# Kernel optimization log

Measured on AMD Instinct MI355X. Metric: run time of the kernel, lower is better.

The kernel has to match this reference:

```python
import jax, jax.numpy as jnp
import numpy as np


def _conv1x1(x, w, b):
    # x: (B,C,H,W), w: (O,C), b: (O,)
    return jnp.einsum('bchw,oc->bohw', x, w) + b[None, :, None, None]


def setup_inputs() -> dict:
    key = jax.random.key(0)
    ks = jax.random.split(key, 10)
    B, C, H, W = 8, 64, 64, 64
    x = jax.random.normal(ks[0], (B, C, H, W), dtype=jnp.float32)
    s = 0.05
    params = {}
    names = ['wq', 'wQ', 'wK', 'wV']
    for i, n in enumerate(names):
        params[n] = jax.random.normal(ks[1 + 2 * i], (C, C), dtype=jnp.float32) * s
        params['b' + n[1:]] = jax.random.normal(ks[2 + 2 * i], (C,), dtype=jnp.float32) * s
    return dict(x=x, wq=params['wq'], bq=params['bq'], wQ=params['wQ'], bQ=params['bQ'],
                wK=params['wK'], bK=params['bK'], wV=params['wV'], bV=params['bV'],
                gamma=jnp.ones((1,), dtype=jnp.float32))


def reference(x, wq, bq, wQ, bQ, wK, bK, wV, bV, gamma):
    B, C, H, W = x.shape
    # q = query_conv(x).view(B,-1,W,H)  (pure reshape, matches torch .view on contiguous tensor)
    q = _conv1x1(x, wq, bq).reshape(B, C, W, H)
    # 2x2 average pool, stride 2
    qp = q.reshape(B, C, W // 2, 2, H // 2, 2).mean(axis=(3, 5))
    q_ = qp.reshape(B, C, (W * H) // 4)          # (B, C, N/4)
    K = _conv1x1(x, wK, bK).reshape(B, C, H * W)  # (B, C, N)
    V = _conv1x1(x, wV, bV).reshape(B, C, H * W)  # (B, C, N)
    # stage 1: pooled queries attend over all keys
    attn1 = jax.nn.softmax(jnp.einsum('bcp,bcn->bpn', q_, K), axis=-1)  # (B, N/4, N)
    out = jnp.einsum('bcn,bpn->bcp', V, attn1)                           # (B, C, N/4)
    # stage 2: full queries attend over pooled anchors
    Q = _conv1x1(x, wQ, bQ).reshape(B, C, H * W)                         # (B, C, N)
    attn2 = jax.nn.softmax(jnp.einsum('bcn,bcp->bnp', Q, q_), axis=-1)   # (B, N, N/4)
    out = jnp.einsum('bcp,bnp->bcn', out, attn2)                         # (B, C, N)
    out = out.reshape(B, C, H, W)
    return gamma * out + x
```

## Files before the change

kernel.cpp:

```cpp
#include <hip/hip_runtime.h>
#include <hip/hip_bf16.h>


typedef float  f32x4  __attribute__((ext_vector_type(4)));
typedef __bf16 bf16x8 __attribute__((ext_vector_type(8)));
typedef __bf16 bf16x4 __attribute__((ext_vector_type(4)));

__device__ __forceinline__ int swz(int ch) { return ch ^ ((ch >> 3) & 7); }

__global__ __launch_bounds__(256) void conv4_kernel(
    const float* __restrict__ x,
    const float* __restrict__ wq, const float* __restrict__ bq,
    const float* __restrict__ wQ, const float* __restrict__ bQ,
    const float* __restrict__ wK, const float* __restrict__ bK,
    const float* __restrict__ wV, const float* __restrict__ bV,
    __bf16* __restrict__ Kt, __bf16* __restrict__ Vc,
    __bf16* __restrict__ Qt, __bf16* __restrict__ qt)
{
  __shared__ float xs[64 * 132];
  __shared__ float wsh[64 * 68];

  const int tid = threadIdx.x;
  const int m   = blockIdx.x >> 8;
  const int b   = (blockIdx.x >> 5) & 7;
  const int rp  = blockIdx.x & 31;
  const int n0  = rp << 7;

  const float* wg = (m == 0) ? wK : (m == 1) ? wV : (m == 2) ? wQ : wq;
  const float* bg = (m == 0) ? bK : (m == 1) ? bV : (m == 2) ? bQ : bq;

  for (int i = tid; i < 64 * 32; i += 256) {
    int c = i >> 5, j = i & 31;
    *(f32x4*)&xs[c * 132 + j * 4] =
        *(const f32x4*)&x[((size_t)(b * 64 + c)) * 4096 + n0 + j * 4];
  }
  for (int i = tid; i < 1024; i += 256) {
    int o = i >> 4, c0 = (i & 15) << 2;
    f32x4 v = *(const f32x4*)&wg[o * 64 + c0];
    wsh[(c0 + 0) * 68 + o] = v[0];
    wsh[(c0 + 1) * 68 + o] = v[1];
    wsh[(c0 + 2) * 68 + o] = v[2];
    wsh[(c0 + 3) * 68 + o] = v[3];
  }
  __syncthreads();

  const int ty = tid >> 4, tx = tid & 15;

  float acc[4][8];
  {
    f32x4 bv = *(const f32x4*)&bg[ty * 4];
#pragma unroll
    for (int i = 0; i < 4; ++i)
#pragma unroll
      for (int j = 0; j < 8; ++j) acc[i][j] = bv[i];
  }

#pragma unroll 4
  for (int c = 0; c < 64; ++c) {
    f32x4 wv = *(const f32x4*)&wsh[c * 68 + ty * 4];
    f32x4 xa = *(const f32x4*)&xs[c * 132 + tx * 8];
    f32x4 xb = *(const f32x4*)&xs[c * 132 + tx * 8 + 4];
#pragma unroll
    for (int i = 0; i < 4; ++i) {
#pragma unroll
      for (int j = 0; j < 4; ++j) {
        acc[i][j]     += wv[i] * xa[j];
        acc[i][j + 4] += wv[i] * xb[j];
      }
    }
  }

  if (m == 0 || m == 2) {
    __bf16* dst = (m == 0) ? Kt : Qt;
#pragma unroll
    for (int j = 0; j < 8; ++j) {
      int n = n0 + tx * 8 + j;
      bf16x4 pk;
#pragma unroll
      for (int i = 0; i < 4; ++i) pk[i] = (__bf16)acc[i][j];
      *(bf16x4*)&dst[((size_t)(b * 4096 + n)) * 64 + ty * 4] = pk;
    }
  } else if (m == 1) {
#pragma unroll
    for (int i = 0; i < 4; ++i) {
      int o = ty * 4 + i;
      bf16x8 pk;
#pragma unroll
      for (int j = 0; j < 8; ++j) pk[j] = (__bf16)acc[i][j];
      *(bf16x8*)&Vc[((size_t)(b * 64 + o)) * 4096 + n0 + tx * 8] = pk;
    }
  } else {
    float pl[4][4];
#pragma unroll
    for (int i = 0; i < 4; ++i)
#pragma unroll
      for (int jj = 0; jj < 4; ++jj)
        pl[i][jj] = acc[i][2 * jj] + acc[i][2 * jj + 1];
#pragma unroll
    for (int i = 0; i < 4; ++i)
#pragma unroll
      for (int jj = 0; jj < 4; ++jj)
        pl[i][jj] += __shfl_xor(pl[i][jj], 8);
    if (tx < 8) {
#pragma unroll
      for (int jj = 0; jj < 4; ++jj) {
        int p = rp * 32 + tx * 4 + jj;
        bf16x4 pk;
#pragma unroll
        for (int i = 0; i < 4; ++i) pk[i] = (__bf16)(0.25f * pl[i][jj]);
        *(bf16x4*)&qt[((size_t)(b * 1024 + p)) * 64 + ty * 4] = pk;
      }
    }
  }
}

template <int NQB, int NKS, int KVLEN>
__global__ __launch_bounds__(512, 2) void attn_part_kernel(
    const __bf16* __restrict__ Qg,
    const __bf16* __restrict__ Kg,
    const __bf16* __restrict__ Vg,
    __bf16* __restrict__ partOb,
    float* __restrict__ partL)
{
  __shared__ __align__(16) char smem[65536];
  constexpr int RND = KVLEN / (NKS * 64);

  const int tid = threadIdx.x;
  const int w = tid >> 6, lane = tid & 63;
  const int lg = (lane >> 4) & 3, lp = lane & 15;
  const int b   = blockIdx.x / (NQB * NKS);
  const int rem = blockIdx.x % (NQB * NKS);
  const int qb  = rem / NKS;
  const int ks  = rem % NKS;

  bf16x8 qf[2][2];
#pragma unroll
  for (int qs = 0; qs < 2; ++qs) {
    const __bf16* qg =
        Qg + ((size_t)(b * (NQB * 256) + qb * 256 + w * 32 + qs * 16 + lp)) * 64;
    qf[qs][0] = *(const bf16x8*)(qg + lg * 8);
    qf[qs][1] = *(const bf16x8*)(qg + 32 + lg * 8);
  }

  f32x4 acc[2][4];
#pragma unroll
  for (int qs = 0; qs < 2; ++qs)
#pragma unroll
    for (int ct = 0; ct < 4; ++ct) acc[qs][ct] = (f32x4){0.f, 0.f, 0.f, 0.f};
  float l_run[2] = {0.f, 0.f};

  bf16x8 kreg, vreg;
  const int swt = swz(tid);
  auto load_tile = [&](int r) {
    const int kv0 = ks * (KVLEN / NKS) + r * 64;
    kreg = *(const bf16x8*)(Kg + ((size_t)(b * KVLEN + kv0 + (tid >> 3))) * 64 +
                            (tid & 7) * 8);
    vreg = *(const bf16x8*)(Vg + ((size_t)(b * 64 + (tid >> 3))) * KVLEN + kv0 +
                            (tid & 7) * 8);
  };
  auto write_tile = [&](int nb) {
    *(bf16x8*)((__bf16*)(smem + nb * 8192) + swt * 8) = kreg;
    *(bf16x8*)((__bf16*)(smem + 16384 + nb * 8192) + swt * 8) = vreg;
  };

  load_tile(0); write_tile(0); load_tile(1);
  __syncthreads();

  for (int r = 0; r < RND; ++r) {
    const int cur = r & 1;
    if (r + 1 < RND) write_tile(cur ^ 1);
    if (r + 2 < RND) load_tile(r + 2);

    const __bf16* lK = (const __bf16*)(smem + cur * 8192);
    const __bf16* lV = (const __bf16*)(smem + 16384 + cur * 8192);
    __bf16* lP = (__bf16*)(smem + 32768) + w * 2048;

    bf16x8 ka[4][2];
#pragma unroll
    for (int mt = 0; mt < 4; ++mt) {
      int ch0 = (mt * 16 + lp) * 8 + lg;
      ka[mt][0] = *(const bf16x8*)(lK + swz(ch0) * 8);
      ka[mt][1] = *(const bf16x8*)(lK + swz(ch0 + 4) * 8);
    }

#pragma unroll
    for (int qs = 0; qs < 2; ++qs) {
      f32x4 S[4];
#pragma unroll
      for (int mt = 0; mt < 4; ++mt) {
        f32x4 z = (f32x4){0.f, 0.f, 0.f, 0.f};
        z = __builtin_amdgcn_mfma_f32_16x16x32_bf16(ka[mt][0], qf[qs][0], z, 0, 0, 0);
        z = __builtin_amdgcn_mfma_f32_16x16x32_bf16(ka[mt][1], qf[qs][1], z, 0, 0, 0);
        S[mt] = z;
      }

      float rs = 0.f;
#pragma unroll
      for (int mt = 0; mt < 4; ++mt)
#pragma unroll
        for (int rr = 0; rr < 4; ++rr) {
          float e = __expf(S[mt][rr]);
          S[mt][rr] = e;
          rs += e;
        }
      rs += __shfl_xor(rs, 16);
      rs += __shfl_xor(rs, 32);
      l_run[qs] += rs;

#pragma unroll
      for (int mt = 0; mt < 4; ++mt) {
        bf16x4 pk;
#pragma unroll
        for (int rr = 0; rr < 4; ++rr) pk[rr] = (__bf16)S[mt][rr];
        int boff = (qs * 16 + lp) * 128 + mt * 32 + lg * 8;
        *(bf16x4*)((char*)lP + (boff ^ ((lp & 7) << 4))) = pk;
      }
    }

    bf16x8 pf[2][2];
#pragma unroll
    for (int qs = 0; qs < 2; ++qs) {
      int chp = (qs * 16 + lp) * 8 + lg;
      pf[qs][0] = *(const bf16x8*)(lP + swz(chp) * 8);
      pf[qs][1] = *(const bf16x8*)(lP + swz(chp + 4) * 8);
    }
#pragma unroll
    for (int ct = 0; ct < 4; ++ct) {
      int chv = (ct * 16 + lp) * 8 + lg;
      bf16x8 v0 = *(const bf16x8*)(lV + swz(chv) * 8);
      bf16x8 v1 = *(const bf16x8*)(lV + swz(chv + 4) * 8);
#pragma unroll
      for (int qs = 0; qs < 2; ++qs) {
        acc[qs][ct] = __builtin_amdgcn_mfma_f32_16x16x32_bf16(v0, pf[qs][0], acc[qs][ct], 0, 0, 0);
        acc[qs][ct] = __builtin_amdgcn_mfma_f32_16x16x32_bf16(v1, pf[qs][1], acc[qs][ct], 0, 0, 0);
      }
    }
    __syncthreads();
  }

  const int gq = w * 32;
  const size_t pbase = (size_t)((b * NQB + qb) * NKS + ks);
  if (lg == 0) {
#pragma unroll
    for (int qs = 0; qs < 2; ++qs)
      partL[pbase * 256 + gq + qs * 16 + lp] = l_run[qs];
  }
  __bf16* po = partOb + pbase * 16384;
#pragma unroll
  for (int qs = 0; qs < 2; ++qs)
#pragma unroll
    for (int ct = 0; ct < 4; ++ct)
#pragma unroll
      for (int rr = 0; rr < 4; ++rr)
        po[(ct * 16 + lg * 4 + rr) * 256 + gq + qs * 16 + lp] =
            (__bf16)acc[qs][ct][rr];
}

__global__ __launch_bounds__(256) void combine1_kernel(
    const __bf16* __restrict__ partOb, const float* __restrict__ partL,
    __bf16* __restrict__ O1)
{
  __shared__ float linv[256];

  const int tid = threadIdx.x;
  const int b   = blockIdx.x >> 5;
  const int qb  = (blockIdx.x >> 3) & 3;
  const int cs  = blockIdx.x & 7;
  const size_t rbase = (size_t)((b * 4 + qb) * 16);

  {
    float l = 0.f;
#pragma unroll
    for (int s = 0; s < 16; ++s) l += partL[(rbase + s) * 256 + tid];
    linv[tid] = 1.0f / l;
  }
  __syncthreads();

  const int c = cs * 8 + (tid >> 5), q8 = (tid & 31) * 8;
  float o[8] = {0.f, 0.f, 0.f, 0.f, 0.f, 0.f, 0.f, 0.f};
#pragma unroll
  for (int s = 0; s < 16; ++s) {
    bf16x8 v = *(const bf16x8*)(partOb + (rbase + s) * 16384 + c * 256 + q8);
#pragma unroll
    for (int j = 0; j < 8; ++j) o[j] += (float)v[j];
  }
  bf16x8 pk;
#pragma unroll
  for (int j = 0; j < 8; ++j) pk[j] = (__bf16)(o[j] * linv[q8 + j]);
  *(bf16x8*)(O1 + ((size_t)(b * 64 + c)) * 1024 + qb * 256 + q8) = pk;
}

__global__ __launch_bounds__(256) void combine2_kernel(
    const __bf16* __restrict__ partOb, const float* __restrict__ partL,
    float* __restrict__ outp, const float* __restrict__ xres,
    const float* __restrict__ gammap)
{
  __shared__ float linv[256];

  const int tid = threadIdx.x;
  const int b   = blockIdx.x >> 7;
  const int qb  = (blockIdx.x >> 3) & 15;
  const int cs  = blockIdx.x & 7;
  const size_t rbase = (size_t)((b * 16 + qb) * 4);

  {
    float l = 0.f;
#pragma unroll
    for (int s = 0; s < 4; ++s) l += partL[(rbase + s) * 256 + tid];
    linv[tid] = 1.0f / l;
  }
  __syncthreads();

  const int c = cs * 8 + (tid >> 5), q8 = (tid & 31) * 8;
  float o[8] = {0.f, 0.f, 0.f, 0.f, 0.f, 0.f, 0.f, 0.f};
#pragma unroll
  for (int s = 0; s < 4; ++s) {
    bf16x8 v = *(const bf16x8*)(partOb + (rbase + s) * 16384 + c * 256 + q8);
#pragma unroll
    for (int j = 0; j < 8; ++j) o[j] += (float)v[j];
  }
  const float g0 = gammap[0];
  const size_t oi = ((size_t)(b * 64 + c)) * 4096 + qb * 256 + q8;
  f32x4 xa = *(const f32x4*)(xres + oi);
  f32x4 xb = *(const f32x4*)(xres + oi + 4);
  f32x4 ra, rb;
#pragma unroll
  for (int j = 0; j < 4; ++j) {
    ra[j] = g0 * (o[j] * linv[q8 + j]) + xa[j];
    rb[j] = g0 * (o[j + 4] * linv[q8 + 4 + j]) + xb[j];
  }
  *(f32x4*)(outp + oi) = ra;
  *(f32x4*)(outp + oi + 4) = rb;
}

extern "C" void kernel_launch(void* const* d_in, const int* in_sizes, int n_in,
                              void* d_out, int out_size, void* d_ws, size_t ws_size,
                              hipStream_t stream) {
  const float* x     = (const float*)d_in[0];
  const float* wq    = (const float*)d_in[1];
  const float* bq    = (const float*)d_in[2];
  const float* wQ    = (const float*)d_in[3];
  const float* bQ    = (const float*)d_in[4];
  const float* wK    = (const float*)d_in[5];
  const float* bK    = (const float*)d_in[6];
  const float* wV    = (const float*)d_in[7];
  const float* bV    = (const float*)d_in[8];
  const float* gamma = (const float*)d_in[9];

  __bf16* ws = (__bf16*)d_ws;
  __bf16* Kt = ws;
  __bf16* Vc = ws + 2097152;
  __bf16* Qt = ws + 4194304;
  __bf16* qt = ws + 6291456;
  __bf16* O1 = ws + 6815744;
  __bf16* partOb1 = (__bf16*)((char*)d_ws + (16ull << 20));
  float*  partL1  = (float*)((char*)d_ws + (33ull << 20));
  __bf16* partOb2 = (__bf16*)((char*)d_ws + (48ull << 20));
  float*  partL2  = (float*)((char*)d_ws + (65ull << 20));

  hipLaunchKernelGGL(conv4_kernel, dim3(1024), dim3(256), 0, stream,
                     x, wq, bq, wQ, bQ, wK, bK, wV, bV, Kt, Vc, Qt, qt);
  hipLaunchKernelGGL((attn_part_kernel<4, 16, 4096>), dim3(512), dim3(512), 0,
                     stream, qt, Kt, Vc, partOb1, partL1);
  hipLaunchKernelGGL(combine1_kernel, dim3(256), dim3(256), 0, stream,
                     partOb1, partL1, O1);
  hipLaunchKernelGGL((attn_part_kernel<16, 4, 1024>), dim3(512), dim3(512), 0,
                     stream, Qt, qt, O1, partOb2, partL2);
  hipLaunchKernelGGL(combine2_kernel, dim3(1024), dim3(256), 0, stream,
                     partOb2, partL2, (float*)d_out, x, gamma);
}
```

Baseline: 75.10 us.

## Load K/V fragments directly from global, fuse stage-2 combine into attention epilogue

The attention kernel no longer stages K and V tiles through double-buffered shared memory with block-wide barriers. Each wave now reads its MFMA operands straight from global memory (relying on L1/L2 caching), and LDS is used only for the per-wave P buffer. Stage 2 drops its KV split: each block covers the whole 1024-long KV range with 4 waves and writes normalized output plus the gamma-scaled residual directly, which removes the combine2 kernel and the partial buffers. The risks are redundant global loads across waves, uncoalesced strided V reads, and lower parallelism in stage 2 (256 blocks of 256 threads), plus scalar, non-vectorized stores to the output.

```diff
diff --git a/kernel.cpp b/kernel.cpp
--- a/kernel.cpp
+++ b/kernel.cpp
@@ -114,16 +114,19 @@
   }
 }
 
-template <int NQB, int NKS, int KVLEN>
-__global__ __launch_bounds__(512, 2) void attn_part_kernel(
+template <int NQB, int NKS, int KVLEN, int NW, bool FINAL>
+__global__ __launch_bounds__(NW * 64, 4) void attn_kernel(
     const __bf16* __restrict__ Qg,
     const __bf16* __restrict__ Kg,
     const __bf16* __restrict__ Vg,
     __bf16* __restrict__ partOb,
-    float* __restrict__ partL)
+    float* __restrict__ partL,
+    float* __restrict__ outp,
+    const float* __restrict__ xres, const float* __restrict__ gammap)
 {
-  __shared__ __align__(16) char smem[65536];
-  constexpr int RND = KVLEN / (NKS * 64);
+  __shared__ __align__(16) char smem[NW * 4096];
+  constexpr int RND = KVLEN / NKS / 64;
+  constexpr int QPB = NW * 32;
 
   const int tid = threadIdx.x;
   const int w = tid >> 6, lane = tid & 63;
@@ -137,7 +140,7 @@
 #pragma unroll
   for (int qs = 0; qs < 2; ++qs) {
     const __bf16* qg =
-        Qg + ((size_t)(b * (NQB * 256) + qb * 256 + w * 32 + qs * 16 + lp)) * 64;
+        Qg + ((size_t)(b * (NQB * QPB) + qb * QPB + w * 32 + qs * 16 + lp)) * 64;
     qf[qs][0] = *(const bf16x8*)(qg + lg * 8);
     qf[qs][1] = *(const bf16x8*)(qg + 32 + lg * 8);
   }
@@ -149,38 +152,19 @@
     for (int ct = 0; ct < 4; ++ct) acc[qs][ct] = (f32x4){0.f, 0.f, 0.f, 0.f};
   float l_run[2] = {0.f, 0.f};
 
-  bf16x8 kreg, vreg;
-  const int swt = swz(tid);
-  auto load_tile = [&](int r) {
+  __bf16* lP = (__bf16*)(smem + w * 4096);
+
+  for (int r = 0; r < RND; ++r) {
     const int kv0 = ks * (KVLEN / NKS) + r * 64;
-    kreg = *(const bf16x8*)(Kg + ((size_t)(b * KVLEN + kv0 + (tid >> 3))) * 64 +
-                            (tid & 7) * 8);
-    vreg = *(const bf16x8*)(Vg + ((size_t)(b * 64 + (tid >> 3))) * KVLEN + kv0 +
-                            (tid & 7) * 8);
-  };
-  auto write_tile = [&](int nb) {
-    *(bf16x8*)((__bf16*)(smem + nb * 8192) + swt * 8) = kreg;
-    *(bf16x8*)((__bf16*)(smem + 16384 + nb * 8192) + swt * 8) = vreg;
-  };
-
-  load_tile(0); write_tile(0); load_tile(1);
-  __syncthreads();
-
-  for (int r = 0; r < RND; ++r) {
-    const int cur = r & 1;
-    if (r + 1 < RND) write_tile(cur ^ 1);
-    if (r + 2 < RND) load_tile(r + 2);
-
-    const __bf16* lK = (const __bf16*)(smem + cur * 8192);
-    const __bf16* lV = (const __bf16*)(smem + 16384 + cur * 8192);
-    __bf16* lP = (__bf16*)(smem + 32768) + w * 2048;
+    const __bf16* kb = Kg + ((size_t)(b * KVLEN + kv0)) * 64;
+    const __bf16* vb = Vg + (size_t)b * 64 * KVLEN + kv0;
 
     bf16x8 ka[4][2];
 #pragma unroll
     for (int mt = 0; mt < 4; ++mt) {
-      int ch0 = (mt * 16 + lp) * 8 + lg;
-      ka[mt][0] = *(const bf16x8*)(lK + swz(ch0) * 8);
-      ka[mt][1] = *(const bf16x8*)(lK + swz(ch0 + 4) * 8);
+      const __bf16* kr = kb + (mt * 16 + lp) * 64 + lg * 8;
+      ka[mt][0] = *(const bf16x8*)(kr);
+      ka[mt][1] = *(const bf16x8*)(kr + 32);
     }
 
 #pragma unroll
@@ -226,34 +210,50 @@
     }
 #pragma unroll
     for (int ct = 0; ct < 4; ++ct) {
-      int chv = (ct * 16 + lp) * 8 + lg;
-      bf16x8 v0 = *(const bf16x8*)(lV + swz(chv) * 8);
-      bf16x8 v1 = *(const bf16x8*)(lV + swz(chv + 4) * 8);
+      const __bf16* vr = vb + (size_t)(ct * 16 + lp) * KVLEN + lg * 8;
+      bf16x8 v0 = *(const bf16x8*)(vr);
+      bf16x8 v1 = *(const bf16x8*)(vr + 32);
 #pragma unroll
       for (int qs = 0; qs < 2; ++qs) {
         acc[qs][ct] = __builtin_amdgcn_mfma_f32_16x16x32_bf16(v0, pf[qs][0], acc[qs][ct], 0, 0, 0);
         acc[qs][ct] = __builtin_amdgcn_mfma_f32_16x16x32_bf16(v1, pf[qs][1], acc[qs][ct], 0, 0, 0);
       }
     }
-    __syncthreads();
-  }
-
-  const int gq = w * 32;
-  const size_t pbase = (size_t)((b * NQB + qb) * NKS + ks);
-  if (lg == 0) {
+  }
+
+  if constexpr (FINAL) {
+    const float g0 = gammap[0];
+#pragma unroll
+    for (int qs = 0; qs < 2; ++qs) {
+      const int nq = qb * QPB + w * 32 + qs * 16 + lp;
+      const float inv = 1.0f / l_run[qs];
+#pragma unroll
+      for (int ct = 0; ct < 4; ++ct)
+#pragma unroll
+        for (int rr = 0; rr < 4; ++rr) {
+          int c = ct * 16 + lg * 4 + rr;
+          size_t oi = ((size_t)(b * 64 + c)) * (NQB * QPB) + nq;
+          outp[oi] = g0 * (acc[qs][ct][rr] * inv) + xres[oi];
+        }
+    }
+  } else {
+    const int gq = w * 32;
+    const size_t pbase = (size_t)((b * NQB + qb) * NKS + ks);
+    if (lg == 0) {
+#pragma unroll
+      for (int qs = 0; qs < 2; ++qs)
+        partL[pbase * QPB + gq + qs * 16 + lp] = l_run[qs];
+    }
+    __bf16* po = partOb + pbase * (64 * QPB);
 #pragma unroll
     for (int qs = 0; qs < 2; ++qs)
-      partL[pbase * 256 + gq + qs * 16 + lp] = l_run[qs];
-  }
-  __bf16* po = partOb + pbase * 16384;
-#pragma unroll
-  for (int qs = 0; qs < 2; ++qs)
-#pragma unroll
-    for (int ct = 0; ct < 4; ++ct)
-#pragma unroll
-      for (int rr = 0; rr < 4; ++rr)
-        po[(ct * 16 + lg * 4 + rr) * 256 + gq + qs * 16 + lp] =
-            (__bf16)acc[qs][ct][rr];
+#pragma unroll
+      for (int ct = 0; ct < 4; ++ct)
+#pragma unroll
+        for (int rr = 0; rr < 4; ++rr)
+          po[(ct * 16 + lg * 4 + rr) * QPB + gq + qs * 16 + lp] =
+              (__bf16)acc[qs][ct][rr];
+  }
 }
 
 __global__ __launch_bounds__(256) void combine1_kernel(
@@ -288,49 +288,6 @@
 #pragma unroll
   for (int j = 0; j < 8; ++j) pk[j] = (__bf16)(o[j] * linv[q8 + j]);
   *(bf16x8*)(O1 + ((size_t)(b * 64 + c)) * 1024 + qb * 256 + q8) = pk;
-}
-
-__global__ __launch_bounds__(256) void combine2_kernel(
-    const __bf16* __restrict__ partOb, const float* __restrict__ partL,
-    float* __restrict__ outp, const float* __restrict__ xres,
-    const float* __restrict__ gammap)
-{
-  __shared__ float linv[256];
-
-  const int tid = threadIdx.x;
-  const int b   = blockIdx.x >> 7;
-  const int qb  = (blockIdx.x >> 3) & 15;
-  const int cs  = blockIdx.x & 7;
-  const size_t rbase = (size_t)((b * 16 + qb) * 4);
-
-  {
-    float l = 0.f;
-#pragma unroll
-    for (int s = 0; s < 4; ++s) l += partL[(rbase + s) * 256 + tid];
-    linv[tid] = 1.0f / l;
-  }
-  __syncthreads();
-
-  const int c = cs * 8 + (tid >> 5), q8 = (tid & 31) * 8;
-  float o[8] = {0.f, 0.f, 0.f, 0.f, 0.f, 0.f, 0.f, 0.f};
-#pragma unroll
-  for (int s = 0; s < 4; ++s) {
-    bf16x8 v = *(const bf16x8*)(partOb + (rbase + s) * 16384 + c * 256 + q8);
-#pragma unroll
-    for (int j = 0; j < 8; ++j) o[j] += (float)v[j];
-  }
-  const float g0 = gammap[0];
-  const size_t oi = ((size_t)(b * 64 + c)) * 4096 + qb * 256 + q8;
-  f32x4 xa = *(const f32x4*)(xres + oi);
-  f32x4 xb = *(const f32x4*)(xres + oi + 4);
-  f32x4 ra, rb;
-#pragma unroll
-  for (int j = 0; j < 4; ++j) {
-    ra[j] = g0 * (o[j] * linv[q8 + j]) + xa[j];
-    rb[j] = g0 * (o[j + 4] * linv[q8 + 4 + j]) + xb[j];
-  }
-  *(f32x4*)(outp + oi) = ra;
-  *(f32x4*)(outp + oi + 4) = rb;
 }
 
 extern "C" void kernel_launch(void* const* d_in, const int* in_sizes, int n_in,
@@ -355,17 +312,16 @@
   __bf16* O1 = ws + 6815744;
   __bf16* partOb1 = (__bf16*)((char*)d_ws + (16ull << 20));
   float*  partL1  = (float*)((char*)d_ws + (33ull << 20));
-  __bf16* partOb2 = (__bf16*)((char*)d_ws + (48ull << 20));
-  float*  partL2  = (float*)((char*)d_ws + (65ull << 20));
 
   hipLaunchKernelGGL(conv4_kernel, dim3(1024), dim3(256), 0, stream,
                      x, wq, bq, wQ, bQ, wK, bK, wV, bV, Kt, Vc, Qt, qt);
-  hipLaunchKernelGGL((attn_part_kernel<4, 16, 4096>), dim3(512), dim3(512), 0,
-                     stream, qt, Kt, Vc, partOb1, partL1);
+  hipLaunchKernelGGL((attn_kernel<4, 16, 4096, 8, false>), dim3(512),
+                     dim3(512), 0, stream, qt, Kt, Vc, partOb1, partL1,
+                     (float*)nullptr, (const float*)nullptr,
+                     (const float*)nullptr);
   hipLaunchKernelGGL(combine1_kernel, dim3(256), dim3(256), 0, stream,
                      partOb1, partL1, O1);
-  hipLaunchKernelGGL((attn_part_kernel<16, 4, 1024>), dim3(512), dim3(512), 0,
-                     stream, Qt, qt, O1, partOb2, partL2);
-  hipLaunchKernelGGL(combine2_kernel, dim3(1024), dim3(256), 0, stream,
-                     partOb2, partL2, (float*)d_out, x, gamma);
+  hipLaunchKernelGGL((attn_kernel<32, 1, 1024, 4, true>), dim3(256),
+                     dim3(256), 0, stream, Qt, qt, O1, (__bf16*)nullptr,
+                     (float*)nullptr, (float*)d_out, x, gamma);
 }
```

Measured after the change: 124.0 us. 1.65x slower.
